# Kernel optimization log

Hardware: AMD Instinct MI355X
Metric: run time of the kernel (lower is better)

The kernel has to match this reference:

```python
import jax, jax.numpy as jnp
import numpy as np

H = 8
HD = 128
D = 1024
SCALE = 0.12
EOT = 50256
LN_EPS = 1e-6
THETA = 1024.0


def _layernorm(x, w):
    mu = jnp.mean(x, axis=-1, keepdims=True)
    var = jnp.mean(jnp.square(x - mu), axis=-1, keepdims=True)
    return (x - mu) * jax.lax.rsqrt(var + LN_EPS) * w


def _rmsnorm(x):
    eps = jnp.finfo(x.dtype).eps
    return x * jax.lax.rsqrt(jnp.mean(jnp.square(x), axis=-1, keepdims=True) + eps)


def _rope_tables(seq_len, head_dim):
    # half-truncated RoPE: only first half of the rotation pairs get nonzero freqs
    n = head_dim // 4
    freqs = (1.0 / THETA) ** jnp.linspace(0.0, 1.0, n)
    ang = jnp.concatenate([freqs, jnp.zeros((n,), freqs.dtype)])  # [head_dim//2]
    th = jnp.arange(seq_len, dtype=jnp.float32)[:, None] * ang[None, :]
    return jnp.cos(th), jnp.sin(th)  # each [S, head_dim//2]


def _apply_rope(x, cos, sin):
    # x: [B, S, H, hd]
    x1, x2 = jnp.split(x, 2, axis=-1)
    c = cos[None, :, None, :]
    s = sin[None, :, None, :]
    return jnp.concatenate([x1 * c + x2 * s, -x1 * s + x2 * c], axis=-1)


def setup_inputs() -> dict:
    key = jax.random.key(0)
    ks = jax.random.split(key, 10)
    B, S = 2, 2048
    return {
        "x": jax.random.normal(ks[0], (B, S, D), jnp.float32),
        "value_embed": jax.random.normal(ks[1], (S, D), jnp.float32),
        "x0": jax.random.normal(ks[2], (B, S, D), jnp.float32),
        "lambdas": jax.random.uniform(ks[3], (2,), jnp.float32),
        "sa_lambdas": jax.random.uniform(ks[4], (2,), jnp.float32),
        "ln1_w": jnp.ones((D,), jnp.float32),
        "ln2_w": jnp.ones((D,), jnp.float32),
        "w_qkv": jax.random.normal(ks[5], (D, 3 * D), jnp.float32) * 0.02,
        "w_o": jax.random.normal(ks[6], (D, D), jnp.float32) * 0.02,
        "w_fc": jax.random.normal(ks[7], (D, 4 * D), jnp.float32) * 0.02,
        "w_proj": jax.random.normal(ks[8], (4 * D, D), jnp.float32) * 0.02,
        "input_ids": jax.random.randint(ks[9], (S,), 0, 50257, jnp.int64),
    }


def reference(x, value_embed, x0, lambdas, sa_lambdas, ln1_w, ln2_w,
              w_qkv, w_o, w_fc, w_proj, input_ids):
    B, S, Dm = x.shape
    # U-Net residual mixing
    x = lambdas[0] * x + lambdas[1] * x0

    # attention branch
    xn = _layernorm(x, ln1_w)
    qkv = xn @ w_qkv                                # [B,S,3D]
    q, k, v = jnp.split(qkv, 3, axis=-1)
    q = q.reshape(B, S, H, HD)
    k = k.reshape(B, S, H, HD)
    v = v.reshape(B, S, H, HD)

    cos, sin = _rope_tables(S, HD)
    q = _apply_rope(q, cos, sin)
    k = _apply_rope(k, cos, sin)

    # value-embedding mixing
    ve = value_embed.reshape(S, H, HD)[None]        # [1,S,H,hd]
    v = sa_lambdas[0] * v + sa_lambdas[1] * ve

    # QK norm (unit-weight RMSNorm)
    q = _rmsnorm(q)
    k = _rmsnorm(k)

    # document-aware causal mask
    docs = jnp.cumsum(input_ids == EOT)
    idx = jnp.arange(S)
    mask = (idx[:, None] >= idx[None, :]) & (docs[:, None] == docs[None, :])

    scores = jnp.einsum("bqhd,bkhd->bhqk", q, k) * SCALE
    scores = jnp.where(mask[None, None], scores, -jnp.inf)
    attn = jax.nn.softmax(scores, axis=-1)
    out = jnp.einsum("bhqk,bkhd->bqhd", attn, v).reshape(B, S, Dm)
    x = x + out @ w_o

    # MLP with relu^2
    xn = _layernorm(x, ln2_w)
    h = jnp.square(jax.nn.relu(xn @ w_fc))
    x = x + h @ w_proj
    return x
```

## Files before the change

kernel.cpp:

```cpp
#include <hip/hip_runtime.h>

#define EOT_ID 50256

typedef __attribute__((ext_vector_type(8))) short bf16x8;
typedef __attribute__((ext_vector_type(4))) float f32x4;
typedef __attribute__((ext_vector_type(4))) unsigned short u16x4;

#define GLOAD_LDS(g, l)                                                        \
  __builtin_amdgcn_global_load_lds(                                            \
      (const __attribute__((address_space(1))) unsigned int*)(g),              \
      (__attribute__((address_space(3))) unsigned int*)(l), 16, 0, 0)

__device__ __forceinline__ unsigned short f2bf(float f) {
  union { float f; unsigned int u; } v; v.f = f;
  unsigned int r = v.u + 0x7FFFu + ((v.u >> 16) & 1u);
  return (unsigned short)(r >> 16);
}
__device__ __forceinline__ float bf2f(unsigned short b) {
  union { unsigned int u; float f; } v; v.u = ((unsigned int)b) << 16;
  return v.f;
}

__global__ void rope_tab_kernel(float* __restrict__ ct, float* __restrict__ st) {
  const int idx = blockIdx.x * 256 + threadIdx.x;
  const int s = idx >> 5, i = idx & 31;
  const float ang = (float)s * exp2f(-10.0f * (float)i / 31.0f);
  float sv, cv;
  sincosf(ang, &sv, &cv);
  ct[idx] = cv;
  st[idx] = sv;
}

__global__ __launch_bounds__(1024)
void docs_kernel(const int* __restrict__ ids, int* __restrict__ qstart) {
  __shared__ int a[2048], b2[2048];
  const int t = threadIdx.x;
  for (int i = t; i < 2048; i += 1024)
    a[i] = (ids[i] == EOT_ID) ? i : 0;
  __syncthreads();
  int* cur = a; int* nxt = b2;
  for (int off = 1; off < 2048; off <<= 1) {
    for (int i = t; i < 2048; i += 1024) {
      int v = cur[i];
      if (i >= off) { int u = cur[i - off]; v = (u > v) ? u : v; }
      nxt[i] = v;
    }
    __syncthreads();
    int* tmp = cur; cur = nxt; nxt = tmp;
  }
  for (int i = t; i < 2048; i += 1024) qstart[i] = cur[i];
}

__global__ __launch_bounds__(256)
void wtrans_kernel(const float* __restrict__ in, unsigned short* __restrict__ out,
                   int K, int N) {
  __shared__ float tile[32][33];
  const int nb = N >> 5;
  const int k0 = (blockIdx.x / nb) << 5, n0 = (blockIdx.x % nb) << 5;
  const int tx = threadIdx.x & 31, ty = threadIdx.x >> 5;
#pragma unroll
  for (int p = 0; p < 4; p++)
    tile[ty + p * 8][tx] = in[(size_t)(k0 + ty + p * 8) * N + n0 + tx];
  __syncthreads();
#pragma unroll
  for (int p = 0; p < 4; p++)
    out[(size_t)(n0 + ty + p * 8) * K + k0 + tx] = f2bf(tile[tx][ty + p * 8]);
}

template<bool MIX>
__global__ __launch_bounds__(256)
void ln_kernel(const float* __restrict__ x, const float* __restrict__ x0,
               const float* __restrict__ lam, const float* __restrict__ w,
               float* __restrict__ xm, unsigned short* __restrict__ xn) {
  __shared__ float red[8];
  const int row = blockIdx.x, t = threadIdx.x;
  const size_t base = (size_t)row << 10;
  float4 v = *(const float4*)(x + base + t * 4);
  if (MIX) {
    const float l0 = lam[0], l1 = lam[1];
    const float4 v0 = *(const float4*)(x0 + base + t * 4);
    v.x = l0 * v.x + l1 * v0.x;
    v.y = l0 * v.y + l1 * v0.y;
    v.z = l0 * v.z + l1 * v0.z;
    v.w = l0 * v.w + l1 * v0.w;
    *(float4*)(xm + base + t * 4) = v;
  }
  float s = v.x + v.y + v.z + v.w;
  float q = v.x * v.x + v.y * v.y + v.z * v.z + v.w * v.w;
#pragma unroll
  for (int off = 1; off < 64; off <<= 1) {
    s += __shfl_xor(s, off);
    q += __shfl_xor(q, off);
  }
  const int wid = t >> 6;
  if ((t & 63) == 0) { red[wid] = s; red[4 + wid] = q; }
  __syncthreads();
  s = red[0] + red[1] + red[2] + red[3];
  q = red[4] + red[5] + red[6] + red[7];
  const float mu = s * (1.0f / 1024.0f);
  const float var = q * (1.0f / 1024.0f) - mu * mu;
  const float rstd = rsqrtf(var + 1e-6f);
  const float4 wv = *(const float4*)(w + t * 4);
  ushort4 u;
  u.x = f2bf((v.x - mu) * rstd * wv.x);
  u.y = f2bf((v.y - mu) * rstd * wv.y);
  u.z = f2bf((v.z - mu) * rstd * wv.z);
  u.w = f2bf((v.w - mu) * rstd * wv.w);
  *(ushort4*)(xn + base + t * 4) = u;
}

template<int EPI, int BM, int BK>
__global__ __launch_bounds__(256, 4)
void gemm_bt(const unsigned short* __restrict__ A,
             const unsigned short* __restrict__ Bt,
             void* __restrict__ Cout,
             const float* __restrict__ res,
             int M, int N, int K) {
  __shared__ unsigned short As[2][BM * BK];
  __shared__ unsigned short Bs[2][128 * BK];
  const int t = threadIdx.x;
  const int wid = t >> 6;
  const int lane = t & 63;
  const int ln = lane & 15, kg = lane >> 4;
  const int nbm = M / BM;
  const int xcd = (int)blockIdx.x & 7, rr = (int)blockIdx.x >> 3;
  const int slab = nbm >> 3;
  const int bm = xcd * slab + (rr % slab);
  const int bn = rr / slab;
  const int m0 = bm * BM, n0 = bn << 7;
  const int wrow = (BM == 128) ? ((wid >> 1) * 64) : 0;
  const int wcol = (BM == 128) ? ((wid & 1) * 64) : (wid * 32);
  constexpr int NJ = (BM == 128) ? 4 : 2;
  constexpr int LA = BM * BK / 2048;
  constexpr int LB = 128 * BK / 2048;
  constexpr int KC = BK / 32;

  f32x4 acc[4][NJ] = {};

  const unsigned short* Abase = A + (size_t)m0 * K;
  const unsigned short* Bbase = Bt + (size_t)n0 * K;

  auto swz = [&](int row, int chunk) -> int {
    if constexpr (BK == 32) return chunk ^ ((row >> 1) & 3);
    else                    return chunk ^ (row & 7);
  };

  auto STAGE = [&](int bb, int kt) {
#pragma unroll
    for (int p = 0; p < LA; p++) {
      const int e = t * 8 + p * 2048;
      const int r = e / BK;
      const int cs = swz(r, (e >> 3) & (BK / 8 - 1));
      GLOAD_LDS(Abase + (size_t)r * K + kt + cs * 8, &As[bb][p * 2048 + wid * 512]);
    }
#pragma unroll
    for (int p = 0; p < LB; p++) {
      const int e = t * 8 + p * 2048;
      const int r = e / BK;
      const int cs = swz(r, (e >> 3) & (BK / 8 - 1));
      GLOAD_LDS(Bbase + (size_t)r * K + kt + cs * 8, &Bs[bb][p * 2048 + wid * 512]);
    }
  };

  STAGE(0, 0);
  int cur = 0;
  const int nk = K / BK;
  for (int ki = 0; ki < nk; ki++) {
    if (ki + 1 < nk) {
      STAGE(cur ^ 1, (ki + 1) * BK);
      if constexpr (LA + LB == 4)
        asm volatile("s_waitcnt vmcnt(4)" ::: "memory");
      else
        asm volatile("s_waitcnt vmcnt(6)" ::: "memory");
    } else {
      asm volatile("s_waitcnt vmcnt(0)" ::: "memory");
    }
    __builtin_amdgcn_s_barrier();

#pragma unroll
    for (int c = 0; c < KC; c++) {
      bf16x8 af[4], bfr[NJ];
#pragma unroll
      for (int i = 0; i < 4; i++) {
        const int ra = wrow + i * 16 + ln;
        af[i] = *(const bf16x8*)(&As[cur][ra * BK + swz(ra, c * 4 + kg) * 8]);
      }
#pragma unroll
      for (int j = 0; j < NJ; j++) {
        const int rb = wcol + j * 16 + ln;
        bfr[j] = *(const bf16x8*)(&Bs[cur][rb * BK + swz(rb, c * 4 + kg) * 8]);
      }
#pragma unroll
      for (int i = 0; i < 4; i++)
#pragma unroll
        for (int j = 0; j < NJ; j++)
          acc[i][j] = __builtin_amdgcn_mfma_f32_16x16x32_bf16(af[i], bfr[j], acc[i][j], 0, 0, 0);
    }

    __builtin_amdgcn_s_barrier();
    cur ^= 1;
  }

#pragma unroll
  for (int i = 0; i < 4; i++) {
#pragma unroll
    for (int j = 0; j < NJ; j++) {
#pragma unroll
      for (int r = 0; r < 4; r++) {
        const int row = m0 + wrow + i * 16 + kg * 4 + r;
        const int col = n0 + wcol + j * 16 + ln;
        const size_t idx = (size_t)row * N + col;
        float v = acc[i][j][r];
        if (EPI == 0) {
          ((float*)Cout)[idx] = v;
        } else if (EPI == 1) {
          ((float*)Cout)[idx] = v + res[idx];
        } else if (EPI == 2) {
          v = fmaxf(v, 0.0f);
          ((unsigned short*)Cout)[idx] = f2bf(v * v);
        } else {
          ((unsigned short*)Cout)[idx] = f2bf(v);
        }
      }
    }
  }
}

__global__ __launch_bounds__(256)
void rope_rms_kernel(const unsigned short* __restrict__ qkv,
                     const float* __restrict__ ct, const float* __restrict__ st,
                     const float* __restrict__ ve, const float* __restrict__ salam,
                     unsigned short* __restrict__ Qh, unsigned short* __restrict__ Kh,
                     unsigned short* __restrict__ Vt) {
  const int t = threadIdx.x;
  const int wid = t >> 6, i = t & 63;
  const int g = blockIdx.x * 4 + wid;
  const int b = g >> 14;
  const int s = (g >> 3) & 2047;
  const int h = g & 7;
  const unsigned short* base = qkv + (size_t)(b * 2048 + s) * 3072 + h * 128;
  float c = 1.0f, sn = 0.0f;
  if (i < 32) { c = ct[s * 32 + i]; sn = st[s * 32 + i]; }
  const float q1 = bf2f(base[i]), q2 = bf2f(base[64 + i]);
  const float k1 = bf2f(base[1024 + i]), k2 = bf2f(base[1024 + 64 + i]);
  const float q1r = q1 * c + q2 * sn, q2r = q2 * c - q1 * sn;
  const float k1r = k1 * c + k2 * sn, k2r = k2 * c - k1 * sn;
  float sq = q1r * q1r + q2r * q2r;
  float sk = k1r * k1r + k2r * k2r;
#pragma unroll
  for (int off = 1; off < 64; off <<= 1) {
    sq += __shfl_xor(sq, off);
    sk += __shfl_xor(sk, off);
  }
  const float eps = 1.1920929e-7f;
  const float rq = rsqrtf(sq * (1.0f / 128.0f) + eps);
  const float rk = rsqrtf(sk * (1.0f / 128.0f) + eps);
  unsigned short* qp = Qh + (((size_t)(b * 2048 + s) * 8 + h) << 7);
  unsigned short* kp = Kh + (((size_t)(b * 2048 + s) * 8 + h) << 7);
  qp[i] = f2bf(q1r * rq); qp[64 + i] = f2bf(q2r * rq);
  kp[i] = f2bf(k1r * rk); kp[64 + i] = f2bf(k2r * rk);
  const float l0 = salam[0], l1 = salam[1];
  const float* vep = ve + (size_t)s * 1024 + h * 128;
  const float v1 = l0 * bf2f(base[2048 + i]) + l1 * vep[i];
  const float v2 = l0 * bf2f(base[2048 + 64 + i]) + l1 * vep[64 + i];
  unsigned short* vp = Vt + (((size_t)(b * 8 + h) * 128) << 11) + s;
  vp[(size_t)i << 11] = f2bf(v1);
  vp[(size_t)(64 + i) << 11] = f2bf(v2);
}

__global__ __launch_bounds__(256, 2)
void attn_kernel(const unsigned short* __restrict__ Qh,
                 const unsigned short* __restrict__ Kh,
                 const unsigned short* __restrict__ Vt,
                 const int* __restrict__ qstart,
                 unsigned short* __restrict__ Out) {
  __shared__ unsigned short Ks[2 * 64 * 128];
  __shared__ unsigned short Vs[2 * 128 * 64];
  __shared__ unsigned short Ps[4][16 * 72];

  const int blk = blockIdx.x;
  const int p_ = blk >> 4;
  const int qt = (p_ < 16) ? (31 - p_) : (p_ - 16);
  const int bh = blk & 15;
  const int b = bh >> 3, h = bh & 7;
  const int q0 = qt << 6;
  const int t = threadIdx.x;
  const int wid = t >> 6, lane = t & 63;
  const int ln = lane & 15, kg = lane >> 4;
  const int qrow = q0 + wid * 16;

  bf16x8 qf[4];
  {
    const unsigned short* qp = Qh + (((size_t)(b * 2048 + qrow + ln) * 8 + h) << 7);
#pragma unroll
    for (int s = 0; s < 4; s++) qf[s] = *(const bf16x8*)(qp + s * 32 + kg * 8);
  }
  const int qid = qrow + ln;
  const int qs = qstart[qid];
  int qsmax = qs;
#pragma unroll
  for (int off = 1; off < 16; off <<= 1)
    qsmax = max(qsmax, __shfl_xor(qsmax, off));

  float m = -64.0f, l = 0.0f;
  f32x4 o[8] = {};

  const int kt0 = qstart[q0] & ~63;
  const int kend = q0 + 64;
  const float SC = 0.12f * 1.4426950408889634f;

  auto STAGE = [&](int bb, int kt) {
#pragma unroll
    for (int r = 0; r < 4; r++) {
      const int e = t * 8 + r * 2048;
      const int row = e >> 7;
      const int scol = (((e >> 3) & 15) ^ (row & 7)) << 3;
      GLOAD_LDS(Kh + (((size_t)(b * 2048 + kt + row) * 8 + h) << 7) + scol,
                &Ks[bb * 8192 + r * 2048 + wid * 512]);
    }
#pragma unroll
    for (int r = 0; r < 4; r++) {
      const int e = t * 8 + r * 2048;
      const int row = e >> 6;
      const int scol = (((e >> 3) & 7) ^ (row & 7)) << 3;
      GLOAD_LDS(Vt + (((size_t)((b * 8 + h) * 128 + row)) << 11) + kt + scol,
                &Vs[bb * 8192 + r * 2048 + wid * 512]);
    }
  };

  STAGE(0, kt0);
  int cur = 0;

  for (int kt = kt0; kt < kend; kt += 64) {
    const bool hasnext = (kt + 64 < kend);
    if (hasnext) {
      STAGE(cur ^ 1, kt + 64);
      asm volatile("s_waitcnt vmcnt(8)" ::: "memory");
    } else {
      asm volatile("s_waitcnt vmcnt(0)" ::: "memory");
    }
    __builtin_amdgcn_s_barrier();

    const unsigned short* ksb = &Ks[cur * 8192];
    const unsigned short* vsb = &Vs[cur * 8192];

    f32x4 sacc[4] = {};
#pragma unroll
    for (int nt = 0; nt < 4; nt++) {
#pragma unroll
      for (int s = 0; s < 4; s++) {
        bf16x8 kf = *(const bf16x8*)(&ksb[(nt * 16 + ln) * 128 + ((((s << 2) + kg) ^ (ln & 7)) << 3)]);
        sacc[nt] = __builtin_amdgcn_mfma_f32_16x16x32_bf16(kf, qf[s], sacc[nt], 0, 0, 0);
      }
    }

    const bool full = (kt + 64 <= qrow) && (kt >= qsmax);

    float p[4][4];
    float mx = -1e30f;
    if (full) {
#pragma unroll
      for (int nt = 0; nt < 4; nt++)
#pragma unroll
        for (int r = 0; r < 4; r++) {
          const float ts = sacc[nt][r] * SC;
          p[nt][r] = ts;
          mx = fmaxf(mx, ts);
        }
    } else {
#pragma unroll
      for (int nt = 0; nt < 4; nt++) {
#pragma unroll
        for (int r = 0; r < 4; r++) {
          const int key = kt + nt * 16 + kg * 4 + r;
          const bool valid = (key <= qid) && (key >= qs);
          const float ts = valid ? sacc[nt][r] * SC : -1e30f;
          p[nt][r] = ts;
          mx = fmaxf(mx, ts);
        }
      }
    }
    mx = fmaxf(mx, __shfl_xor(mx, 16));
    mx = fmaxf(mx, __shfl_xor(mx, 32));

    const bool dresc = __any(mx - m > 8.0f);
    if (dresc) {
      const float mn = fmaxf(m, mx);
      const float fac = exp2f(m - mn);
      m = mn;
      l *= fac;
      float ff[4];
#pragma unroll
      for (int r = 0; r < 4; r++) ff[r] = __shfl(fac, kg * 4 + r);
#pragma unroll
      for (int d = 0; d < 8; d++)
#pragma unroll
        for (int r = 0; r < 4; r++) o[d][r] *= ff[r];
    }

    float sum = 0.0f;
#pragma unroll
    for (int nt = 0; nt < 4; nt++)
#pragma unroll
      for (int r = 0; r < 4; r++) {
        const float pv = exp2f(p[nt][r] - m);
        p[nt][r] = pv;
        sum += pv;
      }
    sum += __shfl_xor(sum, 16);
    sum += __shfl_xor(sum, 32);
    l += sum;

#pragma unroll
    for (int nt = 0; nt < 4; nt++) {
      u16x4 pk;
      pk[0] = f2bf(p[nt][0]); pk[1] = f2bf(p[nt][1]);
      pk[2] = f2bf(p[nt][2]); pk[3] = f2bf(p[nt][3]);
      *(u16x4*)(&Ps[wid][ln * 72 + nt * 16 + kg * 4]) = pk;
    }

#pragma unroll
    for (int ks = 0; ks < 2; ks++) {
      bf16x8 pf = *(const bf16x8*)(&Ps[wid][ln * 72 + ks * 32 + kg * 8]);
#pragma unroll
      for (int d = 0; d < 8; d++) {
        bf16x8 vf = *(const bf16x8*)(&vsb[(d * 16 + ln) * 64 + ((((ks << 2) + kg) ^ (ln & 7)) << 3)]);
        o[d] = __builtin_amdgcn_mfma_f32_16x16x32_bf16(pf, vf, o[d], 0, 0, 0);
      }
    }

    __builtin_amdgcn_s_barrier();
    cur ^= 1;
  }

  const float inv = 1.0f / l;
  float invr[4];
#pragma unroll
  for (int r = 0; r < 4; r++) invr[r] = __shfl(inv, kg * 4 + r);
#pragma unroll
  for (int r = 0; r < 4; r++) {
    const int q = qrow + kg * 4 + r;
#pragma unroll
    for (int d = 0; d < 8; d++) {
      Out[((size_t)(b * 2048 + q) << 10) + h * 128 + d * 16 + ln] = f2bf(o[d][r] * invr[r]);
    }
  }
}

extern "C" void kernel_launch(void* const* d_in, const int* in_sizes, int n_in,
                              void* d_out, int out_size, void* d_ws, size_t ws_size,
                              hipStream_t stream) {
  const float* x     = (const float*)d_in[0];
  const float* vemb  = (const float*)d_in[1];
  const float* x0    = (const float*)d_in[2];
  const float* lam   = (const float*)d_in[3];
  const float* slam  = (const float*)d_in[4];
  const float* ln1w  = (const float*)d_in[5];
  const float* ln2w  = (const float*)d_in[6];
  const float* wqkv  = (const float*)d_in[7];
  const float* wo    = (const float*)d_in[8];
  const float* wfc   = (const float*)d_in[9];
  const float* wproj = (const float*)d_in[10];
  const int*   ids   = (const int*)d_in[11];

  char* ws = (char*)d_ws;
  unsigned short* wqkvT  = (unsigned short*)(ws + 0);
  unsigned short* woT    = (unsigned short*)(ws + 6291456);
  unsigned short* wfcT   = (unsigned short*)(ws + 8388608);
  unsigned short* wprojT = (unsigned short*)(ws + 16777216);
  float*          xm     = (float*)(ws + 25165824);
  unsigned short* qkv    = (unsigned short*)(ws + 41943040);
  unsigned short* hbuf   = (unsigned short*)(ws + 41943040);
  unsigned short* xn1    = (unsigned short*)(ws + 92274688);
  unsigned short* ao     = (unsigned short*)(ws + 92274688);
  unsigned short* qh     = (unsigned short*)(ws + 100663296);
  unsigned short* xn2    = (unsigned short*)(ws + 100663296);
  unsigned short* kh     = (unsigned short*)(ws + 109051904);
  unsigned short* vt     = (unsigned short*)(ws + 117440512);
  float*          x2     = (float*)(ws + 109051904);
  float*          ctab   = (float*)(ws + 125829120);
  float*          stab   = (float*)(ws + 126091264);
  int*            qstart = (int*)(ws + 126353408);

  rope_tab_kernel<<<dim3(256), dim3(256), 0, stream>>>(ctab, stab);
  docs_kernel<<<dim3(1), dim3(1024), 0, stream>>>(ids, qstart);
  wtrans_kernel<<<dim3(32 * 96), dim3(256), 0, stream>>>(wqkv, wqkvT, 1024, 3072);
  wtrans_kernel<<<dim3(32 * 32), dim3(256), 0, stream>>>(wo, woT, 1024, 1024);
  wtrans_kernel<<<dim3(32 * 128), dim3(256), 0, stream>>>(wfc, wfcT, 1024, 4096);
  wtrans_kernel<<<dim3(128 * 32), dim3(256), 0, stream>>>(wproj, wprojT, 4096, 1024);

  ln_kernel<true><<<dim3(4096), dim3(256), 0, stream>>>(x, x0, lam, ln1w, xm, xn1);
  gemm_bt<3, 128, 32><<<dim3(32 * 24), dim3(256), 0, stream>>>(xn1, wqkvT, (void*)qkv,
                                                               (const float*)nullptr, 4096, 3072, 1024);
  rope_rms_kernel<<<dim3(8192), dim3(256), 0, stream>>>(qkv, ctab, stab, vemb, slam, qh, kh, vt);
  attn_kernel<<<dim3(512), dim3(256), 0, stream>>>(qh, kh, vt, qstart, ao);
  gemm_bt<1, 64, 64><<<dim3(64 * 8), dim3(256), 0, stream>>>(ao, woT, (void*)x2, xm, 4096, 1024, 1024);
  ln_kernel<false><<<dim3(4096), dim3(256), 0, stream>>>(x2, (const float*)nullptr,
                                                         (const float*)nullptr, ln2w,
                                                         (float*)nullptr, xn2);
  gemm_bt<2, 128, 32><<<dim3(32 * 32), dim3(256), 0, stream>>>(xn2, wfcT, (void*)hbuf,
                                                               (const float*)nullptr, 4096, 4096, 1024);
  gemm_bt<1, 64, 64><<<dim3(64 * 8), dim3(256), 0, stream>>>(hbuf, wprojT, d_out, x2, 4096, 1024, 4096);
}
```

Baseline: 279.0 us.

## Switch attention to 32x32x16 MFMA with two waves and register-only P transpose

The attention kernel now uses 32x32x16 bf16 MFMA tiles with 2 waves of 32 query rows each (128 threads) instead of 4 waves of 16 rows. The probability matrix is converted to bf16 with v_cvt_pk_bf16_f32 and rearranged across lanes with v_permlane32_swap, which removes the LDS round-trip through the Ps buffer. The LDS swizzle changes to reduce bank conflicts for the new access pattern, and each thread issues more async loads per stage. In exchange there are fewer waves per block and more registers per thread, which may reduce latency hiding.

New measurement: 305.3 us. +9.4%, slower.

```diff
diff --git a/kernel.cpp b/kernel.cpp
--- a/kernel.cpp
+++ b/kernel.cpp
@@ -4,6 +4,7 @@
 
 typedef __attribute__((ext_vector_type(8))) short bf16x8;
 typedef __attribute__((ext_vector_type(4))) float f32x4;
+typedef __attribute__((ext_vector_type(16))) float f32x16;
 typedef __attribute__((ext_vector_type(4))) unsigned short u16x4;
 
 #define GLOAD_LDS(g, l)                                                        \
@@ -20,6 +21,15 @@
   union { unsigned int u; float f; } v; v.u = ((unsigned int)b) << 16;
   return v.f;
 }
+__device__ __forceinline__ unsigned int cvtpk(float lo, float hi) {
+  unsigned int r;
+  asm("v_cvt_pk_bf16_f32 %0, %1, %2" : "=v"(r) : "v"(lo), "v"(hi));
+  return r;
+}
+__device__ __forceinline__ void plswap(unsigned int& a, unsigned int& b) {
+  asm volatile("v_permlane32_swap_b32 %0, %1" : "+v"(a), "+v"(b));
+}
+union U8 { unsigned int u[4]; bf16x8 v; };
 
 __global__ void rope_tab_kernel(float* __restrict__ ct, float* __restrict__ st) {
   const int idx = blockIdx.x * 256 + threadIdx.x;
@@ -268,7 +278,7 @@
   vp[(size_t)(64 + i) << 11] = f2bf(v2);
 }
 
-__global__ __launch_bounds__(256, 2)
+__global__ __launch_bounds__(128, 1)
 void attn_kernel(const unsigned short* __restrict__ Qh,
                  const unsigned short* __restrict__ Kh,
                  const unsigned short* __restrict__ Vt,
@@ -276,7 +286,6 @@
                  unsigned short* __restrict__ Out) {
   __shared__ unsigned short Ks[2 * 64 * 128];
   __shared__ unsigned short Vs[2 * 128 * 64];
-  __shared__ unsigned short Ps[4][16 * 72];
 
   const int blk = blockIdx.x;
   const int p_ = blk >> 4;
@@ -286,24 +295,25 @@
   const int q0 = qt << 6;
   const int t = threadIdx.x;
   const int wid = t >> 6, lane = t & 63;
-  const int ln = lane & 15, kg = lane >> 4;
-  const int qrow = q0 + wid * 16;
-
-  bf16x8 qf[4];
+  const int ln5 = lane & 31, hi = lane >> 5;
+  const int qrow = q0 + wid * 32;
+
+  bf16x8 qf[8];
   {
-    const unsigned short* qp = Qh + (((size_t)(b * 2048 + qrow + ln) * 8 + h) << 7);
-#pragma unroll
-    for (int s = 0; s < 4; s++) qf[s] = *(const bf16x8*)(qp + s * 32 + kg * 8);
-  }
-  const int qid = qrow + ln;
+    const unsigned short* qp =
+        Qh + (((size_t)(b * 2048 + qrow + ln5) * 8 + h) << 7) + hi * 8;
+#pragma unroll
+    for (int ks2 = 0; ks2 < 8; ks2++) qf[ks2] = *(const bf16x8*)(qp + ks2 * 16);
+  }
+  const int qid = qrow + ln5;
   const int qs = qstart[qid];
   int qsmax = qs;
 #pragma unroll
-  for (int off = 1; off < 16; off <<= 1)
+  for (int off = 1; off < 32; off <<= 1)
     qsmax = max(qsmax, __shfl_xor(qsmax, off));
 
   float m = -64.0f, l = 0.0f;
-  f32x4 o[8] = {};
+  f32x16 o[4] = {};
 
   const int kt0 = qstart[q0] & ~63;
   const int kend = q0 + 64;
@@ -311,20 +321,20 @@
 
   auto STAGE = [&](int bb, int kt) {
 #pragma unroll
-    for (int r = 0; r < 4; r++) {
-      const int e = t * 8 + r * 2048;
+    for (int r = 0; r < 8; r++) {
+      const int e = t * 8 + r * 1024;
       const int row = e >> 7;
-      const int scol = (((e >> 3) & 15) ^ (row & 7)) << 3;
-      GLOAD_LDS(Kh + (((size_t)(b * 2048 + kt + row) * 8 + h) << 7) + scol,
-                &Ks[bb * 8192 + r * 2048 + wid * 512]);
-    }
-#pragma unroll
-    for (int r = 0; r < 4; r++) {
-      const int e = t * 8 + r * 2048;
+      const int sc = ((((e >> 3) & 15) ^ ((row ^ (row >> 3)) & 7)) << 3);
+      GLOAD_LDS(Kh + (((size_t)(b * 2048 + kt + row) * 8 + h) << 7) + sc,
+                &Ks[bb * 8192 + r * 1024 + wid * 512]);
+    }
+#pragma unroll
+    for (int r = 0; r < 8; r++) {
+      const int e = t * 8 + r * 1024;
       const int row = e >> 6;
-      const int scol = (((e >> 3) & 7) ^ (row & 7)) << 3;
-      GLOAD_LDS(Vt + (((size_t)((b * 8 + h) * 128 + row)) << 11) + kt + scol,
-                &Vs[bb * 8192 + r * 2048 + wid * 512]);
+      const int sc = ((((e >> 3) & 7) ^ ((row ^ (row >> 3)) & 7)) << 3);
+      GLOAD_LDS(Vt + (((size_t)((b * 8 + h) * 128 + row)) << 11) + kt + sc,
+                &Vs[bb * 8192 + r * 1024 + wid * 512]);
     }
   };
 
@@ -332,10 +342,9 @@
   int cur = 0;
 
   for (int kt = kt0; kt < kend; kt += 64) {
-    const bool hasnext = (kt + 64 < kend);
-    if (hasnext) {
+    if (kt + 64 < kend) {
       STAGE(cur ^ 1, kt + 64);
-      asm volatile("s_waitcnt vmcnt(8)" ::: "memory");
+      asm volatile("s_waitcnt vmcnt(16)" ::: "memory");
     } else {
       asm volatile("s_waitcnt vmcnt(0)" ::: "memory");
     }
@@ -344,43 +353,46 @@
     const unsigned short* ksb = &Ks[cur * 8192];
     const unsigned short* vsb = &Vs[cur * 8192];
 
-    f32x4 sacc[4] = {};
-#pragma unroll
-    for (int nt = 0; nt < 4; nt++) {
-#pragma unroll
-      for (int s = 0; s < 4; s++) {
-        bf16x8 kf = *(const bf16x8*)(&ksb[(nt * 16 + ln) * 128 + ((((s << 2) + kg) ^ (ln & 7)) << 3)]);
-        sacc[nt] = __builtin_amdgcn_mfma_f32_16x16x32_bf16(kf, qf[s], sacc[nt], 0, 0, 0);
-      }
+    f32x16 sacc[2];
+#pragma unroll
+    for (int t2 = 0; t2 < 2; t2++) {
+      f32x16 s = {};
+      const int key = t2 * 32 + ln5;
+      const int kx = (key ^ (key >> 3)) & 7;
+      const unsigned short* krow = &ksb[key * 128];
+#pragma unroll
+      for (int ks2 = 0; ks2 < 8; ks2++) {
+        bf16x8 kf = *(const bf16x8*)(krow + (((2 * ks2 + hi) ^ kx) << 3));
+        s = __builtin_amdgcn_mfma_f32_32x32x16_bf16(kf, qf[ks2], s, 0, 0, 0);
+      }
+      sacc[t2] = s;
     }
 
     const bool full = (kt + 64 <= qrow) && (kt >= qsmax);
 
-    float p[4][4];
+    float p[2][16];
     float mx = -1e30f;
     if (full) {
 #pragma unroll
-      for (int nt = 0; nt < 4; nt++)
-#pragma unroll
-        for (int r = 0; r < 4; r++) {
-          const float ts = sacc[nt][r] * SC;
-          p[nt][r] = ts;
+      for (int t2 = 0; t2 < 2; t2++)
+#pragma unroll
+        for (int i = 0; i < 16; i++) {
+          const float ts = sacc[t2][i] * SC;
+          p[t2][i] = ts;
           mx = fmaxf(mx, ts);
         }
     } else {
 #pragma unroll
-      for (int nt = 0; nt < 4; nt++) {
-#pragma unroll
-        for (int r = 0; r < 4; r++) {
-          const int key = kt + nt * 16 + kg * 4 + r;
+      for (int t2 = 0; t2 < 2; t2++)
+#pragma unroll
+        for (int i = 0; i < 16; i++) {
+          const int key = kt + t2 * 32 + (i & 3) + 8 * (i >> 2) + 4 * hi;
           const bool valid = (key <= qid) && (key >= qs);
-          const float ts = valid ? sacc[nt][r] * SC : -1e30f;
-          p[nt][r] = ts;
+          const float ts = valid ? sacc[t2][i] * SC : -1e30f;
+          p[t2][i] = ts;
           mx = fmaxf(mx, ts);
         }
-      }
-    }
-    mx = fmaxf(mx, __shfl_xor(mx, 16));
+    }
     mx = fmaxf(mx, __shfl_xor(mx, 32));
 
     const bool dresc = __any(mx - m > 8.0f);
@@ -389,43 +401,50 @@
       const float fac = exp2f(m - mn);
       m = mn;
       l *= fac;
-      float ff[4];
-#pragma unroll
-      for (int r = 0; r < 4; r++) ff[r] = __shfl(fac, kg * 4 + r);
-#pragma unroll
-      for (int d = 0; d < 8; d++)
-#pragma unroll
-        for (int r = 0; r < 4; r++) o[d][r] *= ff[r];
+#pragma unroll
+      for (int r = 0; r < 16; r++) {
+        const float fr = __shfl(fac, (r & 3) + 8 * (r >> 2) + 4 * hi);
+        o[0][r] *= fr; o[1][r] *= fr; o[2][r] *= fr; o[3][r] *= fr;
+      }
     }
 
     float sum = 0.0f;
 #pragma unroll
-    for (int nt = 0; nt < 4; nt++)
-#pragma unroll
-      for (int r = 0; r < 4; r++) {
-        const float pv = exp2f(p[nt][r] - m);
-        p[nt][r] = pv;
+    for (int t2 = 0; t2 < 2; t2++)
+#pragma unroll
+      for (int i = 0; i < 16; i++) {
+        const float pv = exp2f(p[t2][i] - m);
+        p[t2][i] = pv;
         sum += pv;
       }
-    sum += __shfl_xor(sum, 16);
     sum += __shfl_xor(sum, 32);
     l += sum;
 
-#pragma unroll
-    for (int nt = 0; nt < 4; nt++) {
-      u16x4 pk;
-      pk[0] = f2bf(p[nt][0]); pk[1] = f2bf(p[nt][1]);
-      pk[2] = f2bf(p[nt][2]); pk[3] = f2bf(p[nt][3]);
-      *(u16x4*)(&Ps[wid][ln * 72 + nt * 16 + kg * 4]) = pk;
-    }
-
-#pragma unroll
-    for (int ks = 0; ks < 2; ks++) {
-      bf16x8 pf = *(const bf16x8*)(&Ps[wid][ln * 72 + ks * 32 + kg * 8]);
-#pragma unroll
-      for (int d = 0; d < 8; d++) {
-        bf16x8 vf = *(const bf16x8*)(&vsb[(d * 16 + ln) * 64 + ((((ks << 2) + kg) ^ (ln & 7)) << 3)]);
-        o[d] = __builtin_amdgcn_mfma_f32_16x16x32_bf16(pf, vf, o[d], 0, 0, 0);
+    bf16x8 pa[4];
+#pragma unroll
+    for (int t2 = 0; t2 < 2; t2++) {
+#pragma unroll
+      for (int bb2 = 0; bb2 < 2; bb2++) {
+        unsigned int a0 = cvtpk(p[t2][bb2 * 8 + 0], p[t2][bb2 * 8 + 1]);
+        unsigned int b0 = cvtpk(p[t2][bb2 * 8 + 4], p[t2][bb2 * 8 + 5]);
+        unsigned int a1 = cvtpk(p[t2][bb2 * 8 + 2], p[t2][bb2 * 8 + 3]);
+        unsigned int b1 = cvtpk(p[t2][bb2 * 8 + 6], p[t2][bb2 * 8 + 7]);
+        plswap(a0, b0);
+        plswap(a1, b1);
+        U8 u; u.u[0] = a0; u.u[1] = a1; u.u[2] = b0; u.u[3] = b1;
+        pa[t2 * 2 + bb2] = u.v;
+      }
+    }
+
+#pragma unroll
+    for (int dt = 0; dt < 4; dt++) {
+      const int d = dt * 32 + ln5;
+      const int dx = (d ^ (d >> 3)) & 7;
+      const unsigned short* vrow = &vsb[d * 64];
+#pragma unroll
+      for (int ks = 0; ks < 4; ks++) {
+        bf16x8 vf = *(const bf16x8*)(vrow + (((2 * ks + hi) ^ dx) << 3));
+        o[dt] = __builtin_amdgcn_mfma_f32_32x32x16_bf16(pa[ks], vf, o[dt], 0, 0, 0);
       }
     }
 
@@ -434,16 +453,15 @@
   }
 
   const float inv = 1.0f / l;
-  float invr[4];
-#pragma unroll
-  for (int r = 0; r < 4; r++) invr[r] = __shfl(inv, kg * 4 + r);
-#pragma unroll
-  for (int r = 0; r < 4; r++) {
-    const int q = qrow + kg * 4 + r;
-#pragma unroll
-    for (int d = 0; d < 8; d++) {
-      Out[((size_t)(b * 2048 + q) << 10) + h * 128 + d * 16 + ln] = f2bf(o[d][r] * invr[r]);
-    }
+#pragma unroll
+  for (int r = 0; r < 16; r++) {
+    const int crow = (r & 3) + 8 * (r >> 2) + 4 * hi;
+    const float ivr = __shfl(inv, crow);
+    const int q = qrow + crow;
+    unsigned short* op = Out + (((size_t)(b * 2048 + q)) << 10) + h * 128 + ln5;
+#pragma unroll
+    for (int dt = 0; dt < 4; dt++)
+      op[dt * 32] = f2bf(o[dt][r] * ivr);
   }
 }
 
@@ -493,7 +511,7 @@
   gemm_bt<3, 128, 32><<<dim3(32 * 24), dim3(256), 0, stream>>>(xn1, wqkvT, (void*)qkv,
                                                                (const float*)nullptr, 4096, 3072, 1024);
   rope_rms_kernel<<<dim3(8192), dim3(256), 0, stream>>>(qkv, ctab, stab, vemb, slam, qh, kh, vt);
-  attn_kernel<<<dim3(512), dim3(256), 0, stream>>>(qh, kh, vt, qstart, ao);
+  attn_kernel<<<dim3(512), dim3(128), 0, stream>>>(qh, kh, vt, qstart, ao);
   gemm_bt<1, 64, 64><<<dim3(64 * 8), dim3(256), 0, stream>>>(ao, woT, (void*)x2, xm, 4096, 1024, 1024);
   ln_kernel<false><<<dim3(4096), dim3(256), 0, stream>>>(x2, (const float*)nullptr,
                                                          (const float*)nullptr, ln2w,
```
